# Kernel optimization log

Hardware: AMD Instinct MI355X
Metric: run time of the kernel (lower is better)

The kernel has to match this reference:

```python
import jax, jax.numpy as jnp
import numpy as np

STRIDE = 1
PAD = 1
KH = KW = 3
KK = KH * KW


def _conv(x, w, b, stride, pad):
    out = jax.lax.conv_general_dilated(
        x, w, (stride, stride), [(pad, pad), (pad, pad)],
        dimension_numbers=('NCHW', 'OIHW', 'NCHW'))
    if b is not None:
        out = out + b[None, :, None, None]
    return out


def _gather(img, yi, xi):
    # img: [B,C,H,W]; yi,xi: [B,KK,Ho,Wo] int32 -> [B,C,KK,Ho,Wo]
    return jax.vmap(lambda im, yy, xx: im[:, yy, xx])(img, yi, xi)


def _deform_conv2d(x, offset, mask, w):
    # Modulated deformable conv v2 (torchvision ops.deform_conv2d semantics,
    # deformable_groups=1, groups=1).
    B, C, H, W = x.shape
    O = w.shape[0]
    Ho, Wo = offset.shape[2], offset.shape[3]
    # offset layout: [B, 2*KK, Ho, Wo], (dy, dx) pairs per kernel tap
    off = offset.reshape(B, KK, 2, Ho, Wo)
    ky = jnp.repeat(jnp.arange(KH, dtype=x.dtype), KW)   # [KK]
    kx = jnp.tile(jnp.arange(KW, dtype=x.dtype), KH)     # [KK]
    oy = jnp.arange(Ho, dtype=x.dtype) * STRIDE - PAD
    ox = jnp.arange(Wo, dtype=x.dtype) * STRIDE - PAD
    py = off[:, :, 0] + ky[None, :, None, None] + oy[None, None, :, None]  # [B,KK,Ho,Wo]
    px = off[:, :, 1] + kx[None, :, None, None] + ox[None, None, None, :]

    y0f = jnp.floor(py); x0f = jnp.floor(px)
    wy1 = py - y0f; wy0 = 1.0 - wy1
    wx1 = px - x0f; wx0 = 1.0 - wx1
    y0 = y0f.astype(jnp.int32); x0 = x0f.astype(jnp.int32)
    y1 = y0 + 1; x1 = x0 + 1

    def corner(yc, xc, wgt):
        valid = ((yc >= 0) & (yc < H) & (xc >= 0) & (xc < W)).astype(x.dtype)
        g = _gather(x, jnp.clip(yc, 0, H - 1), jnp.clip(xc, 0, W - 1))
        return g * (wgt * valid)[:, None]  # [B,C,KK,Ho,Wo]

    sampled = (corner(y0, x0, wy0 * wx0) + corner(y0, x1, wy0 * wx1)
               + corner(y1, x0, wy1 * wx0) + corner(y1, x1, wy1 * wx1))
    # modulate and accumulate with conv weight
    return jnp.einsum('bckhw,bkhw,ock->bohw', sampled, mask,
                      w.reshape(O, C, KK))


def setup_inputs() -> dict:
    key = jax.random.key(0)
    ks = jax.random.split(key, 6)
    B, C, O, H, W = 8, 64, 64, 128, 128
    x = jax.random.normal(ks[0], (B, C, H, W), jnp.float32)
    z = jax.random.normal(ks[1], (B, C, H, W), jnp.float32)
    w_off = jax.random.normal(ks[2], (2 * KK, C, KH, KW), jnp.float32) * 0.01
    b_off = jnp.zeros((2 * KK,), jnp.float32)
    w_mod = jax.random.normal(ks[3], (KK, C, KH, KW), jnp.float32) * 0.01
    b_mod = jnp.zeros((KK,), jnp.float32)
    w_reg = jax.random.normal(ks[4], (O, C, KH, KW), jnp.float32) / np.sqrt(C * KK)
    return dict(x=x, z=z, w_off=w_off, b_off=b_off, w_mod=w_mod,
                b_mod=b_mod, w_reg=w_reg)


def reference(x, z, w_off, b_off, w_mod, b_mod, w_reg):
    offset = _conv(z, w_off, b_off, STRIDE, PAD)                 # [B,2*KK,Ho,Wo]
    mask = 2.0 * jax.nn.sigmoid(_conv(x, w_mod, b_mod, STRIDE, PAD))  # [B,KK,Ho,Wo]
    return _deform_conv2d(x, offset, mask, w_reg)
```

## Files before the change

kernel.cpp:

```cpp
#include <hip/hip_runtime.h>
#include <hip/hip_bf16.h>
#include <math.h>

#define B_  8
#define C_  64
#define O_  64
#define H_  128
#define W_  128
#define HW_ (H_ * W_)

typedef __attribute__((ext_vector_type(8))) short bf16x8;
typedef __attribute__((ext_vector_type(4))) float f32x4;

__device__ __forceinline__ short f2bf(float f) {
    __hip_bfloat16 h = __float2bfloat16(f);
    return *reinterpret_cast<short*>(&h);
}
__device__ __forceinline__ float bf2f(short u) {
    unsigned int v = ((unsigned int)(unsigned short)u) << 16;
    return __uint_as_float(v);
}

__global__ void prep_weights(const float* __restrict__ w_off,
                             const float* __restrict__ w_mod,
                             const float* __restrict__ w_reg,
                             short* __restrict__ wb2,
                             short* __restrict__ wz2,
                             short* __restrict__ wx2) {
    int t = blockIdx.x * blockDim.x + threadIdx.x;
    if (t < 36864) {
        int step = t / 2048, r = t % 2048;
        int mf = r / 512, r2 = r % 512;
        int l = r2 / 32, r3 = r2 % 32;
        int gg = r3 / 8, j = r3 % 8;
        int kt = step >> 1, ch = step & 1;
        int o = mf * 16 + l, c = ch * 32 + gg * 8 + j;
        wb2[t] = f2bf(w_reg[(o * 64 + c) * 9 + kt]);
    }
    if (t < 18432) {
        int step = t / 1024, r = t % 1024;
        int mf = r / 512, r2 = r % 512;
        int l = r2 / 32, r3 = r2 % 32;
        int gg = r3 / 8, j = r3 % 8;
        int kt = step >> 1, ch = step & 1;
        int m = mf * 16 + l, c = ch * 32 + gg * 8 + j;
        wz2[t] = (m < 18) ? f2bf(w_off[(m * 64 + c) * 9 + kt]) : (short)0;
    }
    if (t < 9216) {
        int step = t / 512, r = t % 512;
        int l = r / 32, r3 = r % 32;
        int gg = r3 / 8, j = r3 % 8;
        int kt = step >> 1, ch = step & 1;
        int c = ch * 32 + gg * 8 + j;
        wx2[t] = (l < 9) ? f2bf(w_mod[(l * 64 + c) * 9 + kt]) : (short)0;
    }
}

__global__ __launch_bounds__(256) void to_nhwc(
    const float* __restrict__ x, const float* __restrict__ z,
    unsigned short* __restrict__ xn, unsigned short* __restrict__ zn) {
    __shared__ float t[64 * 65];
    const int bid = blockIdx.x;
    const int xseg = bid & 1;
    const int y = (bid >> 1) & 127;
    const int b = bid >> 8;

#pragma unroll
    for (int arr = 0; arr < 2; ++arr) {
        const float* src = arr ? z : x;
        unsigned short* dst = arr ? zn : xn;
#pragma unroll
        for (int i = 0; i < 16; ++i) {
            int e = threadIdx.x + i * 256;
            int c = e >> 6, px = e & 63;
            t[px * 65 + c] =
                src[((size_t)(b * 64 + c) * H_ + y) * W_ + xseg * 64 + px];
        }
        __syncthreads();
#pragma unroll
        for (int i = 0; i < 2; ++i) {
            int j = threadIdx.x + i * 256;
            int px = j >> 3, q = j & 7;
            bf16x8 v;
#pragma unroll
            for (int jj = 0; jj < 8; ++jj)
                v[jj] = f2bf(t[px * 65 + q * 8 + jj]);
            *(bf16x8*)(dst +
                       ((size_t)((b * H_ + y) * W_ + xseg * 64 + px)) * 64 +
                       q * 8) = v;
        }
        __syncthreads();
    }
}

__device__ __forceinline__ void tap_params2(
    int t, int ho, int pxi, float dy, float dx, float m,
    float& w00, float& w01, float& w10, float& w11,
    int& a00, int& a01, int& a10, int& a11, int& y0u, int& x0u) {
    int ky = t / 3, kx = t - 3 * ky;
    float py = dy + (float)(ky + ho - 1);
    float pxf = dx + (float)(kx + pxi - 1);
    float y0f = floorf(py), x0f = floorf(pxf);
    float wy1 = py - y0f, wy0 = 1.f - wy1;
    float wx1 = pxf - x0f, wx0w = 1.f - wx1;
    int y0 = (int)y0f, x0i = (int)x0f;
    int y1 = y0 + 1, x1 = x0i + 1;
    bool vy0 = (y0 >= 0) && (y0 < H_), vy1 = (y1 >= 0) && (y1 < H_);
    bool vx0 = (x0i >= 0) && (x0i < W_), vx1 = (x1 >= 0) && (x1 < W_);
    w00 = wy0 * wx0w * ((vy0 && vx0) ? m : 0.f);
    w01 = wy0 * wx1 * ((vy0 && vx1) ? m : 0.f);
    w10 = wy1 * wx0w * ((vy1 && vx0) ? m : 0.f);
    w11 = wy1 * wx1 * ((vy1 && vx1) ? m : 0.f);
    int y0c = min(max(y0, 0), H_ - 1), y1c = min(max(y1, 0), H_ - 1);
    int x0c = min(max(x0i, 0), W_ - 1), x1c = min(max(x1, 0), W_ - 1);
    a00 = (y0c * W_ + x0c) * 64;
    a01 = (y0c * W_ + x1c) * 64;
    a10 = (y1c * W_ + x0c) * 64;
    a11 = (y1c * W_ + x1c) * 64;
    y0u = y0;
    x0u = x0i;
}

#define WROW 5
#define WCOL 69
#define PSTR 72

__global__ __launch_bounds__(256, 3) void dcn_fused(
    const unsigned short* __restrict__ zn, const unsigned short* __restrict__ xn,
    const short* __restrict__ wb2, const short* __restrict__ wz2,
    const short* __restrict__ wx2,
    const float* __restrict__ b_off, const float* __restrict__ b_mod,
    float* __restrict__ out)
{
    __shared__ __align__(16) short sx[WROW * WCOL * PSTR];

    const int tid = threadIdx.x;
    const int lane = tid & 63;
    const int wv = tid >> 6;
    const int l15 = lane & 15;
    const int g = lane >> 4;
    const int g8 = g * 8;

    int bid = (int)blockIdx.x;
    bid = (bid & 7) * 256 + (bid >> 3);

    const int pB = bid * 64;
    const int b = pB / HW_;
    const int pixB = pB % HW_;
    const int ho = pixB / W_;
    const int wxB = pixB % W_;
    const int pxi = wv * 16 + l15;

    const unsigned short* znb = zn + (size_t)b * HW_ * 64;
    const unsigned short* xnb = xn + (size_t)b * HW_ * 64;

    for (int t = tid; t < WROW * WCOL * 8; t += 256) {
        int pix = t >> 3, q = t & 7;
        int r = pix / WCOL, c = pix - r * WCOL;
        int gy = min(max(ho - 2 + r, 0), H_ - 1);
        int gx = min(max(wxB - 2 + c, 0), W_ - 1);
        bf16x8 v = *(const bf16x8*)(xnb + (gy * W_ + gx) * 64 + q * 8);
        *(bf16x8*)(sx + pix * PSTR + q * 8) = v;
    }
    __syncthreads();

    f32x4 A0 = {0.f, 0.f, 0.f, 0.f}, A1 = A0, A2 = A0;
    const bf16x8 vzero = {0, 0, 0, 0, 0, 0, 0, 0};

#pragma unroll 1
    for (int kt = 0; kt < 9; ++kt) {
        const int ky = kt / 3, kx = kt - 3 * ky;
        const int iy = ho + ky - 1;
        const int ixg = wxB + pxi + kx - 1;
        const bool v = (iy >= 0) && (iy < H_) && (ixg >= 0) && (ixg < W_);
        const int basez =
            (min(max(iy, 0), H_ - 1) * W_ + min(max(ixg, 0), W_ - 1)) * 64;
        const short* xs = sx + ((ky + 1) * WCOL + pxi + kx + 1) * PSTR;
#pragma unroll
        for (int ch = 0; ch < 2; ++ch) {
            const int step = kt * 2 + ch;
            bf16x8 bz = *(const bf16x8*)(znb + basez + ch * 32 + g8);
            bf16x8 bx = *(const bf16x8*)(xs + (ch * 4 + g) * 8);
            bf16x8 az0 = *(const bf16x8*)(
                wz2 + (size_t)((step * 2 + 0) * 16 + l15) * 32 + g8);
            bf16x8 az1 = *(const bf16x8*)(
                wz2 + (size_t)((step * 2 + 1) * 16 + l15) * 32 + g8);
            bf16x8 ax = *(const bf16x8*)(
                wx2 + (size_t)(step * 16 + l15) * 32 + g8);
            bz = v ? bz : vzero;
            bx = v ? bx : vzero;
            A0 = __builtin_amdgcn_mfma_f32_16x16x32_bf16(az0, bz, A0, 0, 0, 0);
            A1 = __builtin_amdgcn_mfma_f32_16x16x32_bf16(az1, bz, A1, 0, 0, 0);
            A2 = __builtin_amdgcn_mfma_f32_16x16x32_bf16(ax, bx, A2, 0, 0, 0);
        }
    }

#pragma unroll
    for (int r = 0; r < 4; ++r) A0[r] += b_off[g * 4 + r];
    if (g == 0) {
        A1[0] += b_off[16];
        A1[1] += b_off[17];
    }
    float mk0, mk1, mk2, mk3;
    {
        int j0 = g * 4;
        mk0 = 2.f / (1.f + expf(-(A2[0] + b_mod[min(j0 + 0, 8)])));
        mk1 = 2.f / (1.f + expf(-(A2[1] + b_mod[min(j0 + 1, 8)])));
        mk2 = 2.f / (1.f + expf(-(A2[2] + b_mod[min(j0 + 2, 8)])));
        mk3 = 2.f / (1.f + expf(-(A2[3] + b_mod[min(j0 + 3, 8)])));
    }
    auto get_off = [&](int t, float& dy, float& dx, float& m) {
        if (t < 8) {
            float sdy = (t & 1) ? A0[2] : A0[0];
            float sdx = (t & 1) ? A0[3] : A0[1];
            int ln = (t >> 1) * 16 + l15;
            dy = __shfl(sdy, ln, 64);
            dx = __shfl(sdx, ln, 64);
        } else {
            dy = __shfl(A1[0], l15, 64);
            dx = __shfl(A1[1], l15, 64);
        }
        int tb = t & 3;
        float sm = (tb == 0) ? mk0 : (tb == 1) ? mk1 : (tb == 2) ? mk2 : mk3;
        m = __shfl(sm, (t >> 2) * 16 + l15, 64);
    };

    f32x4 D0 = {0.f, 0.f, 0.f, 0.f}, D1 = D0, D2 = D0, D3 = D0;

#pragma unroll 1
    for (int kt = 0; kt < 9; ++kt) {
        float dy, dx, m;
        get_off(kt, dy, dx, m);
        float w00, w01, w10, w11;
        int a00, a01, a10, a11, y0u, x0u;
        tap_params2(kt, ho, wxB + pxi, dy, dx, m, w00, w01, w10, w11, a00,
                    a01, a10, a11, y0u, x0u);

        const bool inw = (y0u >= ho - 2) && (y0u + 1 <= ho + 2) &&
                         (x0u >= wxB - 2) && (x0u + 1 <= wxB + 66);
        bf16x8 c0l, c1l, c2l, c3l, c0h, c1h, c2h, c3h;
        if (__all(inw)) {
            const int pix00 = (y0u - (ho - 2)) * WCOL + (x0u - (wxB - 2));
            const short* p00 = sx + pix00 * PSTR;
            const short* p01 = p00 + PSTR;
            const short* p10 = p00 + WCOL * PSTR;
            const short* p11 = p10 + PSTR;
            c0l = *(const bf16x8*)(p00 + g8);
            c1l = *(const bf16x8*)(p01 + g8);
            c2l = *(const bf16x8*)(p10 + g8);
            c3l = *(const bf16x8*)(p11 + g8);
            c0h = *(const bf16x8*)(p00 + 32 + g8);
            c1h = *(const bf16x8*)(p01 + 32 + g8);
            c2h = *(const bf16x8*)(p10 + 32 + g8);
            c3h = *(const bf16x8*)(p11 + 32 + g8);
        } else {
            c0l = *(const bf16x8*)(xnb + a00 + g8);
            c1l = *(const bf16x8*)(xnb + a01 + g8);
            c2l = *(const bf16x8*)(xnb + a10 + g8);
            c3l = *(const bf16x8*)(xnb + a11 + g8);
            c0h = *(const bf16x8*)(xnb + a00 + 32 + g8);
            c1h = *(const bf16x8*)(xnb + a01 + 32 + g8);
            c2h = *(const bf16x8*)(xnb + a10 + 32 + g8);
            c3h = *(const bf16x8*)(xnb + a11 + 32 + g8);
        }

#pragma unroll
        for (int ch = 0; ch < 2; ++ch) {
            const int step = kt * 2 + ch;
            bf16x8 s0 = ch ? c0h : c0l;
            bf16x8 s1 = ch ? c1h : c1l;
            bf16x8 s2 = ch ? c2h : c2l;
            bf16x8 s3 = ch ? c3h : c3l;
            bf16x8 sv;
#pragma unroll
            for (int j = 0; j < 8; ++j) {
                float s = fmaf(bf2f(s0[j]), w00,
                          fmaf(bf2f(s1[j]), w01,
                          fmaf(bf2f(s2[j]), w10, bf2f(s3[j]) * w11)));
                sv[j] = f2bf(s);
            }
            bf16x8 a0 = *(const bf16x8*)(
                wb2 + (size_t)((step * 4 + 0) * 16 + l15) * 32 + g8);
            bf16x8 a1 = *(const bf16x8*)(
                wb2 + (size_t)((step * 4 + 1) * 16 + l15) * 32 + g8);
            bf16x8 a2 = *(const bf16x8*)(
                wb2 + (size_t)((step * 4 + 2) * 16 + l15) * 32 + g8);
            bf16x8 a3 = *(const bf16x8*)(
                wb2 + (size_t)((step * 4 + 3) * 16 + l15) * 32 + g8);
            D0 = __builtin_amdgcn_mfma_f32_16x16x32_bf16(a0, sv, D0, 0, 0, 0);
            D1 = __builtin_amdgcn_mfma_f32_16x16x32_bf16(a1, sv, D1, 0, 0, 0);
            D2 = __builtin_amdgcn_mfma_f32_16x16x32_bf16(a2, sv, D2, 0, 0, 0);
            D3 = __builtin_amdgcn_mfma_f32_16x16x32_bf16(a3, sv, D3, 0, 0, 0);
        }
    }

#pragma unroll
    for (int mf = 0; mf < 4; ++mf) {
        f32x4 cc = (mf == 0) ? D0 : ((mf == 1) ? D1 : ((mf == 2) ? D2 : D3));
#pragma unroll
        for (int r = 0; r < 4; ++r) {
            const int o = mf * 16 + g * 4 + r;
            out[((size_t)b * O_ + o) * HW_ + pixB + pxi] = cc[r];
        }
    }
}

__global__ __launch_bounds__(256) void deform_fallback(
    const float* __restrict__ x, const float* __restrict__ z,
    const float* __restrict__ w_regp,
    const float* __restrict__ w_off, const float* __restrict__ b_off,
    const float* __restrict__ w_mod, const float* __restrict__ b_mod,
    float* __restrict__ out) {
    int p = blockIdx.x * blockDim.x + threadIdx.x;
    if (p >= B_ * HW_) return;
    int wo = p % W_;
    int ho = (p / W_) % H_;
    int b  = p / HW_;
    int pix = ho * W_ + wo;

    const float* xb = x + (size_t)b * C_ * HW_;

    float accO[18], accM[9];
#pragma unroll
    for (int j = 0; j < 18; ++j) accO[j] = b_off[j];
#pragma unroll
    for (int j = 0; j < 9; ++j) accM[j] = b_mod[j];
    const float* zb = z + (size_t)b * C_ * HW_;
#pragma unroll 1
    for (int c = 0; c < C_; ++c) {
        const float* zc = zb + c * HW_;
        const float* xc = xb + c * HW_;
#pragma unroll
        for (int ky = 0; ky < 3; ++ky) {
            int iy = ho + ky - 1;
            bool vy = (iy >= 0) && (iy < H_);
#pragma unroll
            for (int kx = 0; kx < 3; ++kx) {
                int ix = wo + kx - 1;
                bool v = vy && (ix >= 0) && (ix < W_);
                int k = ky * 3 + kx;
                float zv = v ? zc[iy * W_ + ix] : 0.f;
                float xv = v ? xc[iy * W_ + ix] : 0.f;
#pragma unroll
                for (int j = 0; j < 18; ++j)
                    accO[j] = fmaf(zv, w_off[j * 576 + c * 9 + k], accO[j]);
#pragma unroll
                for (int j = 0; j < 9; ++j)
                    accM[j] = fmaf(xv, w_mod[j * 576 + c * 9 + k], accM[j]);
            }
        }
    }
    float mv[9];
#pragma unroll
    for (int j = 0; j < 9; ++j) mv[j] = 2.f / (1.f + expf(-accM[j]));

    float acc[64];
#pragma unroll
    for (int o = 0; o < 64; ++o) acc[o] = 0.f;

#pragma unroll 1
    for (int k = 0; k < 9; ++k) {
        float dy = accO[2 * k], dx = accO[2 * k + 1], m = mv[k];
        float py = dy + (float)(k / 3 + ho - 1);
        float px = dx + (float)(k % 3 + wo - 1);
        float y0f = floorf(py), x0f = floorf(px);
        float wy1 = py - y0f, wy0 = 1.f - wy1;
        float wx1 = px - x0f, wx0 = 1.f - wx1;
        int y0 = (int)y0f, x0i = (int)x0f;
        int y1 = y0 + 1, x1 = x0i + 1;
        bool vy0 = (y0 >= 0) && (y0 < H_), vy1 = (y1 >= 0) && (y1 < H_);
        bool vx0 = (x0i >= 0) && (x0i < W_), vx1 = (x1 >= 0) && (x1 < W_);
        float w00 = wy0 * wx0 * ((vy0 && vx0) ? m : 0.f);
        float w01 = wy0 * wx1 * ((vy0 && vx1) ? m : 0.f);
        float w10 = wy1 * wx0 * ((vy1 && vx0) ? m : 0.f);
        float w11 = wy1 * wx1 * ((vy1 && vx1) ? m : 0.f);
        int y0c = min(max(y0, 0), H_ - 1), y1c = min(max(y1, 0), H_ - 1);
        int x0c = min(max(x0i, 0), W_ - 1), x1c = min(max(x1, 0), W_ - 1);
        int i00 = y0c * W_ + x0c, i01 = y0c * W_ + x1c;
        int i10 = y1c * W_ + x0c, i11 = y1c * W_ + x1c;
#pragma unroll 1
        for (int c = 0; c < C_; ++c) {
            const float* xc = xb + c * HW_;
            float val = xc[i00] * w00 + xc[i01] * w01 + xc[i10] * w10 +
                        xc[i11] * w11;
            const float* wr = w_regp + c * 9 + k;
#pragma unroll
            for (int o = 0; o < 64; ++o)
                acc[o] = fmaf(val, wr[o * 576], acc[o]);
        }
    }
    float* ob = out + (size_t)b * O_ * HW_ + pix;
#pragma unroll
    for (int o = 0; o < 64; ++o) ob[o * HW_] = acc[o];
}

extern "C" void kernel_launch(void* const* d_in, const int* in_sizes, int n_in,
                              void* d_out, int out_size, void* d_ws,
                              size_t ws_size, hipStream_t stream) {
    const float* x     = (const float*)d_in[0];
    const float* z     = (const float*)d_in[1];
    const float* w_off = (const float*)d_in[2];
    const float* b_off = (const float*)d_in[3];
    const float* w_mod = (const float*)d_in[4];
    const float* b_mod = (const float*)d_in[5];
    const float* w_reg = (const float*)d_in[6];
    float* out = (float*)d_out;

    const size_t need = 129024 + 2 * 16777216ull;

    const int npix = B_ * HW_;
    const int nblk = npix / 64;

    if (ws_size >= need) {
        short* wb2 = (short*)d_ws;
        short* wz2 = wb2 + 36864;
        short* wx2 = wz2 + 18432;
        unsigned short* xn = (unsigned short*)((char*)d_ws + 129024);
        unsigned short* zn = xn + 8388608;

        prep_weights<<<144, 256, 0, stream>>>(w_off, w_mod, w_reg, wb2, wz2,
                                              wx2);
        to_nhwc<<<2048, 256, 0, stream>>>(x, z, xn, zn);
        dcn_fused<<<nblk, 256, 0, stream>>>(zn, xn, wb2, wz2, wx2, b_off,
                                            b_mod, out);
    } else {
        deform_fallback<<<(npix + 255) / 256, 256, 0, stream>>>(
            x, z, w_reg, w_off, b_off, w_mod, b_mod, out);
    }
}
```

Measured before the change: 127.2 us.

## Switch fused DCN to 32x32 MFMA with XOR-swizzled LDS and wave-specialized offset/mask

Replaces the 16x16x32 MFMA tiles with 32x32x16 MFMA in both the offset/mask convolution and the main deformable GEMM, and re-lays out the prepared weights to match. The z neighbourhood is now staged in LDS alongside x, both using an XOR swizzle instead of row padding to avoid bank conflicts. Two waves compute offsets and two compute masks, writing through a shared soff buffer instead of cross-lane shuffles. The extra LDS lowers the occupancy hint from 3 to 2 blocks per CU, which could reduce latency hiding.

Measured after the change: 152.4 us. 1.2x slower.

```diff
diff --git a/kernel.cpp b/kernel.cpp
--- a/kernel.cpp
+++ b/kernel.cpp
@@ -11,6 +11,7 @@
 
 typedef __attribute__((ext_vector_type(8))) short bf16x8;
 typedef __attribute__((ext_vector_type(4))) float f32x4;
+typedef __attribute__((ext_vector_type(16))) float f32x16;
 
 __device__ __forceinline__ short f2bf(float f) {
     __hip_bfloat16 h = __float2bfloat16(f);
@@ -24,35 +25,27 @@
 __global__ void prep_weights(const float* __restrict__ w_off,
                              const float* __restrict__ w_mod,
                              const float* __restrict__ w_reg,
-                             short* __restrict__ wb2,
-                             short* __restrict__ wz2,
-                             short* __restrict__ wx2) {
+                             short* __restrict__ wb3,
+                             short* __restrict__ wza,
+                             short* __restrict__ wxa) {
     int t = blockIdx.x * blockDim.x + threadIdx.x;
     if (t < 36864) {
-        int step = t / 2048, r = t % 2048;
-        int mf = r / 512, r2 = r % 512;
-        int l = r2 / 32, r3 = r2 % 32;
-        int gg = r3 / 8, j = r3 % 8;
-        int kt = step >> 1, ch = step & 1;
-        int o = mf * 16 + l, c = ch * 32 + gg * 8 + j;
-        wb2[t] = f2bf(w_reg[(o * 64 + c) * 9 + kt]);
+        int s = t / 1024, r = t % 1024;
+        int m = r / 512, r2 = r % 512;
+        int ln = r2 / 8, j = r2 % 8;
+        int o = m * 32 + (ln & 31);
+        int tap = s >> 2;
+        int ch = (s & 3) * 16 + (ln >> 5) * 8 + j;
+        wb3[t] = f2bf(w_reg[(o * 64 + ch) * 9 + tap]);
     }
     if (t < 18432) {
-        int step = t / 1024, r = t % 1024;
-        int mf = r / 512, r2 = r % 512;
-        int l = r2 / 32, r3 = r2 % 32;
-        int gg = r3 / 8, j = r3 % 8;
-        int kt = step >> 1, ch = step & 1;
-        int m = mf * 16 + l, c = ch * 32 + gg * 8 + j;
-        wz2[t] = (m < 18) ? f2bf(w_off[(m * 64 + c) * 9 + kt]) : (short)0;
-    }
-    if (t < 9216) {
-        int step = t / 512, r = t % 512;
-        int l = r / 32, r3 = r % 32;
-        int gg = r3 / 8, j = r3 % 8;
-        int kt = step >> 1, ch = step & 1;
-        int c = ch * 32 + gg * 8 + j;
-        wx2[t] = (l < 9) ? f2bf(w_mod[(l * 64 + c) * 9 + kt]) : (short)0;
+        int s = t / 512, r2 = t % 512;
+        int ln = r2 / 8, j = r2 % 8;
+        int row = ln & 31;
+        int tap = s >> 2;
+        int ch = (s & 3) * 16 + (ln >> 5) * 8 + j;
+        wza[t] = (row < 18) ? f2bf(w_off[(row * 64 + ch) * 9 + tap]) : (short)0;
+        wxa[t] = (row < 9) ? f2bf(w_mod[(row * 64 + ch) * 9 + tap]) : (short)0;
     }
 }
 
@@ -123,23 +116,25 @@
 
 #define WROW 5
 #define WCOL 69
-#define PSTR 72
-
-__global__ __launch_bounds__(256, 3) void dcn_fused(
+#define ZROW 3
+#define ZCOL 66
+
+__global__ __launch_bounds__(256, 2) void dcn_fused(
     const unsigned short* __restrict__ zn, const unsigned short* __restrict__ xn,
-    const short* __restrict__ wb2, const short* __restrict__ wz2,
-    const short* __restrict__ wx2,
+    const short* __restrict__ wb3, const short* __restrict__ wza,
+    const short* __restrict__ wxa,
     const float* __restrict__ b_off, const float* __restrict__ b_mod,
     float* __restrict__ out)
 {
-    __shared__ __align__(16) short sx[WROW * WCOL * PSTR];
+    __shared__ __align__(16) short sx[WROW * WCOL * 64];
+    __shared__ __align__(16) short sz[ZROW * ZCOL * 64];
+    __shared__ float soff[27][64];
 
     const int tid = threadIdx.x;
     const int lane = tid & 63;
     const int wv = tid >> 6;
-    const int l15 = lane & 15;
-    const int g = lane >> 4;
-    const int g8 = g * 8;
+    const int l31 = lane & 31;
+    const int kh = lane >> 5;
 
     int bid = (int)blockIdx.x;
     bid = (bid & 7) * 256 + (bid >> 3);
@@ -149,7 +144,6 @@
     const int pixB = pB % HW_;
     const int ho = pixB / W_;
     const int wxB = pixB % W_;
-    const int pxi = wv * 16 + l15;
 
     const unsigned short* znb = zn + (size_t)b * HW_ * 64;
     const unsigned short* xnb = xn + (size_t)b * HW_ * 64;
@@ -159,149 +153,132 @@
         int r = pix / WCOL, c = pix - r * WCOL;
         int gy = min(max(ho - 2 + r, 0), H_ - 1);
         int gx = min(max(wxB - 2 + c, 0), W_ - 1);
-        bf16x8 v = *(const bf16x8*)(xnb + (gy * W_ + gx) * 64 + q * 8);
-        *(bf16x8*)(sx + pix * PSTR + q * 8) = v;
+        int qs = q ^ (pix & 7);
+        *(bf16x8*)(sx + pix * 64 + q * 8) =
+            *(const bf16x8*)(xnb + (gy * W_ + gx) * 64 + qs * 8);
+    }
+    const bf16x8 vzero = {0, 0, 0, 0, 0, 0, 0, 0};
+    for (int t = tid; t < ZROW * ZCOL * 8; t += 256) {
+        int pix = t >> 3, q = t & 7;
+        int r = pix / ZCOL, c = pix - r * ZCOL;
+        int gy = ho - 1 + r, gx = wxB - 1 + c;
+        int qs = q ^ (pix & 7);
+        bf16x8 v = vzero;
+        if (gy >= 0 && gy < H_ && gx >= 0 && gx < W_)
+            v = *(const bf16x8*)(znb + (gy * W_ + gx) * 64 + qs * 8);
+        *(bf16x8*)(sz + pix * 64 + q * 8) = v;
     }
     __syncthreads();
 
-    f32x4 A0 = {0.f, 0.f, 0.f, 0.f}, A1 = A0, A2 = A0;
-    const bf16x8 vzero = {0, 0, 0, 0, 0, 0, 0, 0};
-
-#pragma unroll 1
-    for (int kt = 0; kt < 9; ++kt) {
-        const int ky = kt / 3, kx = kt - 3 * ky;
-        const int iy = ho + ky - 1;
-        const int ixg = wxB + pxi + kx - 1;
-        const bool v = (iy >= 0) && (iy < H_) && (ixg >= 0) && (ixg < W_);
-        const int basez =
-            (min(max(iy, 0), H_ - 1) * W_ + min(max(ixg, 0), W_ - 1)) * 64;
-        const short* xs = sx + ((ky + 1) * WCOL + pxi + kx + 1) * PSTR;
-#pragma unroll
-        for (int ch = 0; ch < 2; ++ch) {
-            const int step = kt * 2 + ch;
-            bf16x8 bz = *(const bf16x8*)(znb + basez + ch * 32 + g8);
-            bf16x8 bx = *(const bf16x8*)(xs + (ch * 4 + g) * 8);
-            bf16x8 az0 = *(const bf16x8*)(
-                wz2 + (size_t)((step * 2 + 0) * 16 + l15) * 32 + g8);
-            bf16x8 az1 = *(const bf16x8*)(
-                wz2 + (size_t)((step * 2 + 1) * 16 + l15) * 32 + g8);
-            bf16x8 ax = *(const bf16x8*)(
-                wx2 + (size_t)(step * 16 + l15) * 32 + g8);
-            bz = v ? bz : vzero;
-            bx = v ? bx : vzero;
-            A0 = __builtin_amdgcn_mfma_f32_16x16x32_bf16(az0, bz, A0, 0, 0, 0);
-            A1 = __builtin_amdgcn_mfma_f32_16x16x32_bf16(az1, bz, A1, 0, 0, 0);
-            A2 = __builtin_amdgcn_mfma_f32_16x16x32_bf16(ax, bx, A2, 0, 0, 0);
-        }
-    }
-
-#pragma unroll
-    for (int r = 0; r < 4; ++r) A0[r] += b_off[g * 4 + r];
-    if (g == 0) {
-        A1[0] += b_off[16];
-        A1[1] += b_off[17];
-    }
-    float mk0, mk1, mk2, mk3;
-    {
-        int j0 = g * 4;
-        mk0 = 2.f / (1.f + expf(-(A2[0] + b_mod[min(j0 + 0, 8)])));
-        mk1 = 2.f / (1.f + expf(-(A2[1] + b_mod[min(j0 + 1, 8)])));
-        mk2 = 2.f / (1.f + expf(-(A2[2] + b_mod[min(j0 + 2, 8)])));
-        mk3 = 2.f / (1.f + expf(-(A2[3] + b_mod[min(j0 + 3, 8)])));
-    }
-    auto get_off = [&](int t, float& dy, float& dx, float& m) {
-        if (t < 8) {
-            float sdy = (t & 1) ? A0[2] : A0[0];
-            float sdx = (t & 1) ? A0[3] : A0[1];
-            int ln = (t >> 1) * 16 + l15;
-            dy = __shfl(sdy, ln, 64);
-            dx = __shfl(sdx, ln, 64);
+    const bool isMask = (wv >= 2);
+    const int pxw = (wv & 1) * 32 + l31;
+
+    f32x16 A;
+#pragma unroll
+    for (int i = 0; i < 16; ++i) A[i] = 0.f;
+
+    if (!isMask) {
+#pragma unroll 1
+        for (int s = 0; s < 36; ++s) {
+            const int t = s >> 2;
+            const int ky = t / 3, kx = t - 3 * ky;
+            const int qq = (s & 3) * 2 + kh;
+            const int zpix = ky * ZCOL + pxw + kx;
+            bf16x8 bfrag =
+                *(const bf16x8*)(sz + zpix * 64 + ((qq ^ (zpix & 7)) << 3));
+            bf16x8 afrag = *(const bf16x8*)(wza + (size_t)(s * 64 + lane) * 8);
+            A = __builtin_amdgcn_mfma_f32_32x32x16_bf16(afrag, bfrag, A, 0, 0,
+                                                        0);
+        }
+    } else {
+#pragma unroll 1
+        for (int s = 0; s < 36; ++s) {
+            const int t = s >> 2;
+            const int ky = t / 3, kx = t - 3 * ky;
+            const int qq = (s & 3) * 2 + kh;
+            const int wpix = (ky + 1) * WCOL + pxw + kx + 1;
+            bf16x8 bfrag =
+                *(const bf16x8*)(sx + wpix * 64 + ((qq ^ (wpix & 7)) << 3));
+            const int iy = ho + ky - 1;
+            const int ixg = wxB + pxw + kx - 1;
+            const bool v = (iy >= 0) && (iy < H_) && (ixg >= 0) && (ixg < W_);
+            bfrag = v ? bfrag : vzero;
+            bf16x8 afrag = *(const bf16x8*)(wxa + (size_t)(s * 64 + lane) * 8);
+            A = __builtin_amdgcn_mfma_f32_32x32x16_bf16(afrag, bfrag, A, 0, 0,
+                                                        0);
+        }
+    }
+
+#pragma unroll
+    for (int reg = 0; reg < 16; ++reg) {
+        const int j = (reg & 3) + 8 * (reg >> 2) + 4 * kh;
+        if (!isMask) {
+            if (j < 18) soff[j][pxw] = A[reg] + b_off[j];
         } else {
-            dy = __shfl(A1[0], l15, 64);
-            dx = __shfl(A1[1], l15, 64);
-        }
-        int tb = t & 3;
-        float sm = (tb == 0) ? mk0 : (tb == 1) ? mk1 : (tb == 2) ? mk2 : mk3;
-        m = __shfl(sm, (t >> 2) * 16 + l15, 64);
-    };
-
-    f32x4 D0 = {0.f, 0.f, 0.f, 0.f}, D1 = D0, D2 = D0, D3 = D0;
-
-#pragma unroll 1
-    for (int kt = 0; kt < 9; ++kt) {
-        float dy, dx, m;
-        get_off(kt, dy, dx, m);
+            if (j < 9)
+                soff[18 + j][pxw] =
+                    2.f / (1.f + expf(-(A[reg] + b_mod[j])));
+        }
+    }
+    __syncthreads();
+
+    const int mB = wv & 1;
+    const int pxb = (wv >> 1) * 32 + l31;
+
+    f32x16 D;
+#pragma unroll
+    for (int i = 0; i < 16; ++i) D[i] = 0.f;
+
+#pragma unroll 1
+    for (int t = 0; t < 9; ++t) {
+        float dy = soff[2 * t][pxb];
+        float dx = soff[2 * t + 1][pxb];
+        float m = soff[18 + t][pxb];
         float w00, w01, w10, w11;
         int a00, a01, a10, a11, y0u, x0u;
-        tap_params2(kt, ho, wxB + pxi, dy, dx, m, w00, w01, w10, w11, a00,
-                    a01, a10, a11, y0u, x0u);
-
+        tap_params2(t, ho, wxB + pxb, dy, dx, m, w00, w01, w10, w11, a00, a01,
+                    a10, a11, y0u, x0u);
         const bool inw = (y0u >= ho - 2) && (y0u + 1 <= ho + 2) &&
                          (x0u >= wxB - 2) && (x0u + 1 <= wxB + 66);
-        bf16x8 c0l, c1l, c2l, c3l, c0h, c1h, c2h, c3h;
-        if (__all(inw)) {
-            const int pix00 = (y0u - (ho - 2)) * WCOL + (x0u - (wxB - 2));
-            const short* p00 = sx + pix00 * PSTR;
-            const short* p01 = p00 + PSTR;
-            const short* p10 = p00 + WCOL * PSTR;
-            const short* p11 = p10 + PSTR;
-            c0l = *(const bf16x8*)(p00 + g8);
-            c1l = *(const bf16x8*)(p01 + g8);
-            c2l = *(const bf16x8*)(p10 + g8);
-            c3l = *(const bf16x8*)(p11 + g8);
-            c0h = *(const bf16x8*)(p00 + 32 + g8);
-            c1h = *(const bf16x8*)(p01 + 32 + g8);
-            c2h = *(const bf16x8*)(p10 + 32 + g8);
-            c3h = *(const bf16x8*)(p11 + 32 + g8);
-        } else {
-            c0l = *(const bf16x8*)(xnb + a00 + g8);
-            c1l = *(const bf16x8*)(xnb + a01 + g8);
-            c2l = *(const bf16x8*)(xnb + a10 + g8);
-            c3l = *(const bf16x8*)(xnb + a11 + g8);
-            c0h = *(const bf16x8*)(xnb + a00 + 32 + g8);
-            c1h = *(const bf16x8*)(xnb + a01 + 32 + g8);
-            c2h = *(const bf16x8*)(xnb + a10 + 32 + g8);
-            c3h = *(const bf16x8*)(xnb + a11 + 32 + g8);
-        }
-
-#pragma unroll
-        for (int ch = 0; ch < 2; ++ch) {
-            const int step = kt * 2 + ch;
-            bf16x8 s0 = ch ? c0h : c0l;
-            bf16x8 s1 = ch ? c1h : c1l;
-            bf16x8 s2 = ch ? c2h : c2l;
-            bf16x8 s3 = ch ? c3h : c3l;
+        const bool allw = __all(inw);
+        int p00 = 0;
+        if (allw) p00 = (y0u - (ho - 2)) * WCOL + (x0u - (wxB - 2));
+        const int p01 = p00 + 1, p10 = p00 + WCOL, p11 = p10 + 1;
+
+#pragma unroll
+        for (int ss = 0; ss < 4; ++ss) {
+            const int s = t * 4 + ss;
+            const int qq = ss * 2 + kh;
+            bf16x8 c0, c1, c2, c3;
+            if (allw) {
+                c0 = *(const bf16x8*)(sx + p00 * 64 + ((qq ^ (p00 & 7)) << 3));
+                c1 = *(const bf16x8*)(sx + p01 * 64 + ((qq ^ (p01 & 7)) << 3));
+                c2 = *(const bf16x8*)(sx + p10 * 64 + ((qq ^ (p10 & 7)) << 3));
+                c3 = *(const bf16x8*)(sx + p11 * 64 + ((qq ^ (p11 & 7)) << 3));
+            } else {
+                c0 = *(const bf16x8*)(xnb + a00 + qq * 8);
+                c1 = *(const bf16x8*)(xnb + a01 + qq * 8);
+                c2 = *(const bf16x8*)(xnb + a10 + qq * 8);
+                c3 = *(const bf16x8*)(xnb + a11 + qq * 8);
+            }
             bf16x8 sv;
 #pragma unroll
             for (int j = 0; j < 8; ++j) {
-                float s = fmaf(bf2f(s0[j]), w00,
-                          fmaf(bf2f(s1[j]), w01,
-                          fmaf(bf2f(s2[j]), w10, bf2f(s3[j]) * w11)));
-                sv[j] = f2bf(s);
+                float s_ = fmaf(bf2f(c0[j]), w00,
+                           fmaf(bf2f(c1[j]), w01,
+                           fmaf(bf2f(c2[j]), w10, bf2f(c3[j]) * w11)));
+                sv[j] = f2bf(s_);
             }
-            bf16x8 a0 = *(const bf16x8*)(
-                wb2 + (size_t)((step * 4 + 0) * 16 + l15) * 32 + g8);
-            bf16x8 a1 = *(const bf16x8*)(
-                wb2 + (size_t)((step * 4 + 1) * 16 + l15) * 32 + g8);
-            bf16x8 a2 = *(const bf16x8*)(
-                wb2 + (size_t)((step * 4 + 2) * 16 + l15) * 32 + g8);
-            bf16x8 a3 = *(const bf16x8*)(
-                wb2 + (size_t)((step * 4 + 3) * 16 + l15) * 32 + g8);
-            D0 = __builtin_amdgcn_mfma_f32_16x16x32_bf16(a0, sv, D0, 0, 0, 0);
-            D1 = __builtin_amdgcn_mfma_f32_16x16x32_bf16(a1, sv, D1, 0, 0, 0);
-            D2 = __builtin_amdgcn_mfma_f32_16x16x32_bf16(a2, sv, D2, 0, 0, 0);
-            D3 = __builtin_amdgcn_mfma_f32_16x16x32_bf16(a3, sv, D3, 0, 0, 0);
-        }
-    }
-
-#pragma unroll
-    for (int mf = 0; mf < 4; ++mf) {
-        f32x4 cc = (mf == 0) ? D0 : ((mf == 1) ? D1 : ((mf == 2) ? D2 : D3));
-#pragma unroll
-        for (int r = 0; r < 4; ++r) {
-            const int o = mf * 16 + g * 4 + r;
-            out[((size_t)b * O_ + o) * HW_ + pixB + pxi] = cc[r];
-        }
+            bf16x8 afrag =
+                *(const bf16x8*)(wb3 + (size_t)((s * 2 + mB) * 64 + lane) * 8);
+            D = __builtin_amdgcn_mfma_f32_32x32x16_bf16(afrag, sv, D, 0, 0, 0);
+        }
+    }
+
+#pragma unroll
+    for (int reg = 0; reg < 16; ++reg) {
+        const int o = mB * 32 + (reg & 3) + 8 * (reg >> 2) + 4 * kh;
+        out[((size_t)b * O_ + o) * HW_ + pixB + pxb] = D[reg];
     }
 }
 
@@ -406,22 +383,22 @@
     const float* w_reg = (const float*)d_in[6];
     float* out = (float*)d_out;
 
-    const size_t need = 129024 + 2 * 16777216ull;
+    const size_t need = 147456 + 2 * 16777216ull;
 
     const int npix = B_ * HW_;
     const int nblk = npix / 64;
 
     if (ws_size >= need) {
-        short* wb2 = (short*)d_ws;
-        short* wz2 = wb2 + 36864;
-        short* wx2 = wz2 + 18432;
-        unsigned short* xn = (unsigned short*)((char*)d_ws + 129024);
+        short* wb3 = (short*)d_ws;
+        short* wza = wb3 + 36864;
+        short* wxa = wza + 18432;
+        unsigned short* xn = (unsigned short*)((char*)d_ws + 147456);
         unsigned short* zn = xn + 8388608;
 
-        prep_weights<<<144, 256, 0, stream>>>(w_off, w_mod, w_reg, wb2, wz2,
-                                              wx2);
+        prep_weights<<<144, 256, 0, stream>>>(w_off, w_mod, w_reg, wb3, wza,
+                                              wxa);
         to_nhwc<<<2048, 256, 0, stream>>>(x, z, xn, zn);
-        dcn_fused<<<nblk, 256, 0, stream>>>(zn, xn, wb2, wz2, wx2, b_off,
+        dcn_fused<<<nblk, 256, 0, stream>>>(zn, xn, wb3, wza, wxa, b_off,
                                             b_mod, out);
     } else {
         deform_fallback<<<(npix + 255) / 256, 256, 0, stream>>>(
```

## Process two output rows per block with 512 threads to share the x halo tile

Applied to the files above, without the earlier changes.

Each block now covers a 2x64 pixel tile with 512 threads (8 waves) instead of 1x64 with 256. The shared-memory x window grows from 5 to 6 rows, so the halo rows loaded per output row drop from 5 to 3, cutting redundant global loads and block count. The launch bounds change to 512 threads with 4 blocks per CU, which tightens the per-thread register budget and may cause spills. The fast-path window check is extended to match the taller tile.

Result: faster. 123.6 us (-2.8%).

```diff
diff --git a/kernel.cpp b/kernel.cpp
--- a/kernel.cpp
+++ b/kernel.cpp
@@ -94,11 +94,11 @@
 }
 
 __device__ __forceinline__ void tap_params2(
-    int t, int ho, int pxi, float dy, float dx, float m,
+    int t, int hop, int pxi, float dy, float dx, float m,
     float& w00, float& w01, float& w10, float& w11,
     int& a00, int& a01, int& a10, int& a11, int& y0u, int& x0u) {
     int ky = t / 3, kx = t - 3 * ky;
-    float py = dy + (float)(ky + ho - 1);
+    float py = dy + (float)(ky + hop - 1);
     float pxf = dx + (float)(kx + pxi - 1);
     float y0f = floorf(py), x0f = floorf(pxf);
     float wy1 = py - y0f, wy0 = 1.f - wy1;
@@ -121,11 +121,11 @@
     x0u = x0i;
 }
 
-#define WROW 5
+#define WROW 6
 #define WCOL 69
 #define PSTR 72
 
-__global__ __launch_bounds__(256, 3) void dcn_fused(
+__global__ __launch_bounds__(512, 4) void dcn_fused(
     const unsigned short* __restrict__ zn, const unsigned short* __restrict__ xn,
     const short* __restrict__ wb2, const short* __restrict__ wz2,
     const short* __restrict__ wx2,
@@ -142,22 +142,26 @@
     const int g8 = g * 8;
 
     int bid = (int)blockIdx.x;
-    bid = (bid & 7) * 256 + (bid >> 3);
-
-    const int pB = bid * 64;
-    const int b = pB / HW_;
-    const int pixB = pB % HW_;
-    const int ho = pixB / W_;
-    const int wxB = pixB % W_;
+    bid = (bid & 7) * 128 + (bid >> 3);
+
+    const int b = bid >> 7;
+    const int rem = bid & 127;
+    const int hoB = (rem >> 1) << 1;
+    const int wxB = (rem & 1) << 6;
+
     const int pxi = wv * 16 + l15;
+    const int rowr = pxi >> 6;
+    const int col = pxi & 63;
+    const int hop = hoB + rowr;
+    const int colg = wxB + col;
 
     const unsigned short* znb = zn + (size_t)b * HW_ * 64;
     const unsigned short* xnb = xn + (size_t)b * HW_ * 64;
 
-    for (int t = tid; t < WROW * WCOL * 8; t += 256) {
+    for (int t = tid; t < WROW * WCOL * 8; t += 512) {
         int pix = t >> 3, q = t & 7;
         int r = pix / WCOL, c = pix - r * WCOL;
-        int gy = min(max(ho - 2 + r, 0), H_ - 1);
+        int gy = min(max(hoB - 2 + r, 0), H_ - 1);
         int gx = min(max(wxB - 2 + c, 0), W_ - 1);
         bf16x8 v = *(const bf16x8*)(xnb + (gy * W_ + gx) * 64 + q * 8);
         *(bf16x8*)(sx + pix * PSTR + q * 8) = v;
@@ -170,12 +174,13 @@
 #pragma unroll 1
     for (int kt = 0; kt < 9; ++kt) {
         const int ky = kt / 3, kx = kt - 3 * ky;
-        const int iy = ho + ky - 1;
-        const int ixg = wxB + pxi + kx - 1;
+        const int iy = hop + ky - 1;
+        const int ixg = colg + kx - 1;
         const bool v = (iy >= 0) && (iy < H_) && (ixg >= 0) && (ixg < W_);
         const int basez =
             (min(max(iy, 0), H_ - 1) * W_ + min(max(ixg, 0), W_ - 1)) * 64;
-        const short* xs = sx + ((ky + 1) * WCOL + pxi + kx + 1) * PSTR;
+        const short* xs =
+            sx + ((rowr + ky + 1) * WCOL + col + kx + 1) * PSTR;
 #pragma unroll
         for (int ch = 0; ch < 2; ++ch) {
             const int step = kt * 2 + ch;
@@ -233,14 +238,14 @@
         get_off(kt, dy, dx, m);
         float w00, w01, w10, w11;
         int a00, a01, a10, a11, y0u, x0u;
-        tap_params2(kt, ho, wxB + pxi, dy, dx, m, w00, w01, w10, w11, a00,
+        tap_params2(kt, hop, colg, dy, dx, m, w00, w01, w10, w11, a00,
                     a01, a10, a11, y0u, x0u);
 
-        const bool inw = (y0u >= ho - 2) && (y0u + 1 <= ho + 2) &&
+        const bool inw = (y0u >= hoB - 2) && (y0u + 1 <= hoB + 3) &&
                          (x0u >= wxB - 2) && (x0u + 1 <= wxB + 66);
         bf16x8 c0l, c1l, c2l, c3l, c0h, c1h, c2h, c3h;
         if (__all(inw)) {
-            const int pix00 = (y0u - (ho - 2)) * WCOL + (x0u - (wxB - 2));
+            const int pix00 = (y0u - (hoB - 2)) * WCOL + (x0u - (wxB - 2));
             const short* p00 = sx + pix00 * PSTR;
             const short* p01 = p00 + PSTR;
             const short* p10 = p00 + WCOL * PSTR;
@@ -294,13 +299,14 @@
         }
     }
 
+    const int pixo = hop * W_ + colg;
 #pragma unroll
     for (int mf = 0; mf < 4; ++mf) {
         f32x4 cc = (mf == 0) ? D0 : ((mf == 1) ? D1 : ((mf == 2) ? D2 : D3));
 #pragma unroll
         for (int r = 0; r < 4; ++r) {
             const int o = mf * 16 + g * 4 + r;
-            out[((size_t)b * O_ + o) * HW_ + pixB + pxi] = cc[r];
+            out[((size_t)b * O_ + o) * HW_ + pixo] = cc[r];
         }
     }
 }
@@ -409,7 +415,7 @@
     const size_t need = 129024 + 2 * 16777216ull;
 
     const int npix = B_ * HW_;
-    const int nblk = npix / 64;
+    const int nblk = npix / 128;
 
     if (ws_size >= need) {
         short* wb2 = (short*)d_ws;
@@ -421,7 +427,7 @@
         prep_weights<<<144, 256, 0, stream>>>(w_off, w_mod, w_reg, wb2, wz2,
                                               wx2);
         to_nhwc<<<2048, 256, 0, stream>>>(x, z, xn, zn);
-        dcn_fused<<<nblk, 256, 0, stream>>>(zn, xn, wb2, wz2, wx2, b_off,
+        dcn_fused<<<nblk, 512, 0, stream>>>(zn, xn, wb2, wz2, wx2, b_off,
                                             b_mod, out);
     } else {
         deform_fallback<<<(npix + 255) / 256, 256, 0, stream>>>(
```
